# Optimization experiments

Hardware: AMD Instinct MI355X
Metric: run time of the kernel (lower is better)

The kernel has to match this reference:

```python
import jax, jax.numpy as jnp
import numpy as np

B, S, D = 4, 2048, 1024
H = 16
HD = D // H  # 64


def _xavier(key, shape):
    fan_in, fan_out = shape[1], shape[0]
    limit = float(np.sqrt(6.0 / (fan_in + fan_out)))
    return jax.random.uniform(key, shape, jnp.float32, -limit, limit)


def setup_inputs() -> dict:
    key = jax.random.key(0)
    ks = jax.random.split(key, 5)
    x = jax.random.normal(ks[0], (B, S, D), dtype=jnp.float32)
    # nn.Linear weights are [out, in]; biases zero-initialized
    Wq = _xavier(ks[1], (D, D)); bq = jnp.zeros((D,), jnp.float32)
    Wk = _xavier(ks[2], (D, D)); bk = jnp.zeros((D,), jnp.float32)
    Wv = _xavier(ks[3], (D, D)); bv = jnp.zeros((D,), jnp.float32)
    Wo = _xavier(ks[4], (D, D)); bo = jnp.zeros((D,), jnp.float32)
    return {"x": x, "Wq": Wq, "bq": bq, "Wk": Wk, "bk": bk,
            "Wv": Wv, "bv": bv, "Wo": Wo, "bo": bo}


def reference(x, Wq, bq, Wk, bk, Wv, bv, Wo, bo):
    # Projections (torch Linear: y = x @ W.T + b), reshape to [B, H, S, HD]
    def proj(W, b):
        y = jnp.einsum('bsd,ed->bse', x, W) + b
        return y.reshape(B, S, H, HD).transpose(0, 2, 1, 3)

    q = proj(Wq, bq)
    k = proj(Wk, bk)
    v = proj(Wv, bv)

    scale = 1.0 / jnp.sqrt(jnp.float32(HD))
    scores = jnp.einsum('bhqd,bhkd->bhqk', q, k) * scale  # [B,H,S,S]
    probs = jax.nn.softmax(scores, axis=-1)
    ctx = jnp.einsum('bhqk,bhkd->bhqd', probs, v)  # [B,H,S,HD]
    ctx = ctx.transpose(0, 2, 1, 3).reshape(B, S, D)
    out = jnp.einsum('bsd,ed->bse', ctx, Wo) + bo
    return out
```

## Files before the change

### kernel.cpp

```cpp
#include <hip/hip_runtime.h>
#include <hip/hip_bf16.h>
#include <stdint.h>


typedef __bf16 bf16;
typedef __bf16 bf16x8 __attribute__((ext_vector_type(8)));
typedef __bf16 bf16x4 __attribute__((ext_vector_type(4)));
typedef float  f32x4  __attribute__((ext_vector_type(4)));

#define MFMA_BF16(A, B, C) __builtin_amdgcn_mfma_f32_16x16x32_bf16(A, B, C, 0, 0, 0)
#define EXP2F(x) __builtin_amdgcn_exp2f(x)

#define ASYNC_CP16(DST_LDS, SRC_G)                                            \
  __builtin_amdgcn_global_load_lds(                                           \
      (__attribute__((address_space(1))) void*)(SRC_G),                       \
      (__attribute__((address_space(3))) void*)(DST_LDS), 16, 0, 0)

__global__ __launch_bounds__(256) void cvt5(
    const float* __restrict__ s0, bf16* __restrict__ d0, int n0,
    const float* __restrict__ s1, bf16* __restrict__ d1, int n1,
    const float* __restrict__ s2, bf16* __restrict__ d2, int n2,
    const float* __restrict__ s3, bf16* __restrict__ d3, int n3,
    const float* __restrict__ s4, bf16* __restrict__ d4, int n4)
{
  const float* s; bf16* d; int n;
  switch (blockIdx.y) {
    case 0: s = s0; d = d0; n = n0; break;
    case 1: s = s1; d = d1; n = n1; break;
    case 2: s = s2; d = d2; n = n2; break;
    case 3: s = s3; d = d3; n = n3; break;
    default: s = s4; d = d4; n = n4; break;
  }
  const int stride = gridDim.x * blockDim.x * 4;
  for (int i = (blockIdx.x * blockDim.x + threadIdx.x) * 4; i < n; i += stride) {
    const float4 v = *(const float4*)(s + i);
    bf16x4 o;
    o[0] = (bf16)v.x; o[1] = (bf16)v.y; o[2] = (bf16)v.z; o[3] = (bf16)v.w;
    *(bf16x4*)(d + i) = o;
  }
}

__global__ __launch_bounds__(256, 4) void gemm_qkv(
    const bf16* __restrict__ X,
    const bf16* __restrict__ Wq, const bf16* __restrict__ Wk,
    const bf16* __restrict__ Wv,
    const float* __restrict__ bq, const float* __restrict__ bk,
    const float* __restrict__ bv,
    bf16* __restrict__ Qo, bf16* __restrict__ Ko, bf16* __restrict__ Vo,
    float qscale)
{
  constexpr int N = 1024, K = 1024;
  __shared__ alignas(16) bf16 As[8192];
  __shared__ alignas(16) bf16 Bs[8192];

  const int sel = blockIdx.x >> 3;
  const bf16*  W    = (sel == 0) ? Wq : (sel == 1) ? Wk : Wv;
  const float* bias = (sel == 0) ? bq : (sel == 1) ? bk : bv;
  bf16*        Y    = (sel == 0) ? Qo : (sel == 1) ? Ko : Vo;
  const float scale = (sel == 0) ? qscale : 1.0f;

  const int tid  = threadIdx.x;
  const int lane = tid & 63;
  const int wv   = tid >> 6;
  const int l15  = lane & 15;
  const int quad = lane >> 4;
  const int wm   = (wv >> 1) * 64;
  const int wn   = (wv & 1) * 64;
  const int nbase = (blockIdx.x & 7) * 128;
  const int mbase = blockIdx.y * 128;

  f32x4 acc[4][4];
  #pragma unroll
  for (int i = 0; i < 4; ++i)
    #pragma unroll
    for (int j = 0; j < 4; ++j)
      acc[i][j] = (f32x4){0.f, 0.f, 0.f, 0.f};

  const int r8 = lane >> 3;
  const int oc = (lane & 7) ^ r8;
  const size_t lrowA = (size_t)(mbase + wv * 32 + r8);
  const size_t lrowB = (size_t)(nbase + wv * 32 + r8);

  for (int kb = 0; kb < K; kb += 64) {
    #pragma unroll
    for (int c = 0; c < 4; ++c) {
      ASYNC_CP16(As + (wv * 32 + c * 8) * 64, X + (lrowA + c * 8) * K + kb + oc * 8);
      ASYNC_CP16(Bs + (wv * 32 + c * 8) * 64, W + (lrowB + c * 8) * K + kb + oc * 8);
    }
    __syncthreads();
    #pragma unroll
    for (int ks = 0; ks < 2; ++ks) {
      bf16x8 af[4], bfr[4];
      #pragma unroll
      for (int t = 0; t < 4; ++t) {
        const int ma = wm + t * 16 + l15;
        af[t]  = *(const bf16x8*)(As + (ma * 8 + ((ks * 4 + quad) ^ (ma & 7))) * 8);
        const int nb = wn + t * 16 + l15;
        bfr[t] = *(const bf16x8*)(Bs + (nb * 8 + ((ks * 4 + quad) ^ (nb & 7))) * 8);
      }
      #pragma unroll
      for (int i = 0; i < 4; ++i)
        #pragma unroll
        for (int j = 0; j < 4; ++j)
          acc[i][j] = MFMA_BF16(af[i], bfr[j], acc[i][j]);
    }
    __syncthreads();
  }

  #pragma unroll
  for (int i = 0; i < 4; ++i) {
    const int row0 = mbase + wm + i * 16 + quad * 4;
    #pragma unroll
    for (int j = 0; j < 4; ++j) {
      const int col = nbase + wn + j * 16 + l15;
      const float bv2 = bias[col];
      #pragma unroll
      for (int r = 0; r < 4; ++r) {
        const float v = (acc[i][j][r] + bv2) * scale;
        const int row = row0 + r;
        if (sel != 2) {
          Y[(size_t)row * N + col] = (bf16)v;
        } else {
          const int bb = row >> 11, s  = row & 2047;
          const int hh = col >> 6,  hd = col & 63;
          Y[(size_t)(bb * 16 + hh) * (2048 * 64) + (size_t)(s >> 6) * 4096 +
            hd * 64 + (s & 63)] = (bf16)v;
        }
      }
    }
  }
}

__global__ __launch_bounds__(256) void gemm_o(
    const bf16* __restrict__ X, const bf16* __restrict__ W,
    const float* __restrict__ bias, float* __restrict__ Yf)
{
  constexpr int N = 1024, K = 1024;
  __shared__ alignas(16) bf16 As[8192];
  __shared__ alignas(16) bf16 Bs[8192];

  const int tid  = threadIdx.x;
  const int lane = tid & 63;
  const int wv   = tid >> 6;
  const int l15  = lane & 15;
  const int quad = lane >> 4;
  const int wm   = (wv >> 1) * 64;
  const int wn   = (wv & 1) * 64;
  const int nbase = blockIdx.x * 128;
  const int mbase = blockIdx.y * 128;

  f32x4 acc[4][4];
  #pragma unroll
  for (int i = 0; i < 4; ++i)
    #pragma unroll
    for (int j = 0; j < 4; ++j)
      acc[i][j] = (f32x4){0.f, 0.f, 0.f, 0.f};

  const int r8 = lane >> 3;
  const int oc = (lane & 7) ^ r8;
  const size_t lrowA = (size_t)(mbase + wv * 32 + r8);
  const size_t lrowB = (size_t)(nbase + wv * 32 + r8);

  for (int kb = 0; kb < K; kb += 64) {
    #pragma unroll
    for (int c = 0; c < 4; ++c) {
      ASYNC_CP16(As + (wv * 32 + c * 8) * 64, X + (lrowA + c * 8) * K + kb + oc * 8);
      ASYNC_CP16(Bs + (wv * 32 + c * 8) * 64, W + (lrowB + c * 8) * K + kb + oc * 8);
    }
    __syncthreads();
    #pragma unroll
    for (int ks = 0; ks < 2; ++ks) {
      bf16x8 af[4], bfr[4];
      #pragma unroll
      for (int t = 0; t < 4; ++t) {
        const int ma = wm + t * 16 + l15;
        af[t]  = *(const bf16x8*)(As + (ma * 8 + ((ks * 4 + quad) ^ (ma & 7))) * 8);
        const int nb = wn + t * 16 + l15;
        bfr[t] = *(const bf16x8*)(Bs + (nb * 8 + ((ks * 4 + quad) ^ (nb & 7))) * 8);
      }
      #pragma unroll
      for (int i = 0; i < 4; ++i)
        #pragma unroll
        for (int j = 0; j < 4; ++j)
          acc[i][j] = MFMA_BF16(af[i], bfr[j], acc[i][j]);
    }
    __syncthreads();
  }

  #pragma unroll
  for (int i = 0; i < 4; ++i) {
    const int row0 = mbase + wm + i * 16 + quad * 4;
    #pragma unroll
    for (int j = 0; j < 4; ++j) {
      const int col = nbase + wn + j * 16 + l15;
      const float bv2 = bias[col];
      #pragma unroll
      for (int r = 0; r < 4; ++r)
        Yf[(size_t)(row0 + r) * N + col] = acc[i][j][r] + bv2;
    }
  }
}

__global__ __launch_bounds__(256, 4) void attn(
    const bf16* __restrict__ Qb, const bf16* __restrict__ Kb,
    const bf16* __restrict__ Vt, bf16* __restrict__ Ob)
{
  constexpr int S = 2048, D = 1024;
  __shared__ alignas(16) bf16 Ks[2][4096];
  __shared__ alignas(16) bf16 Vs[2][4096];

  const int tid  = threadIdx.x;
  const int lane = tid & 63;
  const int wv   = tid >> 6;
  const int l15  = lane & 15;
  const int q0   = lane >> 4;
  const int b = blockIdx.z, h = blockIdx.y;
  const int qblk = blockIdx.x * 128 + wv * 32;

  bf16x8 qf[2][2];
  #pragma unroll
  for (int qt = 0; qt < 2; ++qt)
    #pragma unroll
    for (int dh = 0; dh < 2; ++dh)
      qf[qt][dh] = *(const bf16x8*)(
          Qb + (size_t)(b * S + qblk + qt * 16 + l15) * D + h * 64 + dh * 32 + q0 * 8);

  float lrun[2] = {0.f, 0.f};
  f32x4 o[4][2];
  #pragma unroll
  for (int ht = 0; ht < 4; ++ht)
    #pragma unroll
    for (int qt = 0; qt < 2; ++qt)
      o[ht][qt] = (f32x4){0.f, 0.f, 0.f, 0.f};

  const int r8a = lane >> 3;
  const int oc1 = (lane & 7) ^ (r8a & 3);
  const int oc2 = oc1 ^ 4;
  const int ov  = (lane & 7) ^ r8a;
  const bf16* kgw = Kb + (size_t)(b * S) * D + h * 64 + (size_t)(16 * wv) * D;
  const bf16* vgw = Vt + (size_t)(b * 16 + h) * (2048 * 64) + (16 * wv) * 64;

#define STAGE(KC, BUF)                                                        \
  {                                                                           \
    const bf16* ks = kgw + (size_t)(KC) * D;                                  \
    ASYNC_CP16(&Ks[BUF][wv * 1024],       ks + (size_t)r8a * D + oc1 * 8);    \
    ASYNC_CP16(&Ks[BUF][wv * 1024 + 512], ks + (size_t)(8 + r8a) * D + oc2 * 8);\
    const bf16* vs = vgw + (KC) * 64;                                         \
    ASYNC_CP16(&Vs[BUF][wv * 1024],       vs + r8a * 64 + ov * 8);            \
    ASYNC_CP16(&Vs[BUF][wv * 1024 + 512], vs + (8 + r8a) * 64 + ov * 8);      \
  }

  const int kla = 8 * (l15 >> 2) + (l15 & 3);
  const int swa = (l15 & 3) | (((l15 >> 2) & 1) << 2);
  const int swv = l15 & 7;

  STAGE(0, 0);

  for (int kc = 0, it = 0; kc < S; kc += 64, ++it) {
    const int cur = it & 1;
    __syncthreads();
    if (kc + 64 < S) STAGE(kc + 64, cur ^ 1);

    f32x4 sc[2][4];
    #pragma unroll
    for (int kt = 0; kt < 4; ++kt) {
      const int key = kla + 4 * (kt & 1) + 32 * (kt >> 1);
      const bf16x8 kf0 = *(const bf16x8*)(&Ks[cur][(key * 8 + (q0 ^ swa)) * 8]);
      const bf16x8 kf1 = *(const bf16x8*)(&Ks[cur][(key * 8 + ((q0 + 4) ^ swa)) * 8]);
      #pragma unroll
      for (int qt = 0; qt < 2; ++qt) {
        f32x4 s = MFMA_BF16(kf0, qf[qt][0], ((f32x4){0.f, 0.f, 0.f, 0.f}));
        sc[qt][kt] = MFMA_BF16(kf1, qf[qt][1], s);
      }
    }

    bf16x8 pb[2][2];
    #pragma unroll
    for (int qt = 0; qt < 2; ++qt) {
      float ps = 0.f;
      #pragma unroll
      for (int kt = 0; kt < 4; ++kt)
        #pragma unroll
        for (int r = 0; r < 4; ++r) {
          const float p = EXP2F(sc[qt][kt][r]);
          ps += p;
          pb[qt][kt >> 1][(kt & 1) * 4 + r] = (bf16)p;
        }
      lrun[qt] += ps;
    }

    #pragma unroll
    for (int ht = 0; ht < 4; ++ht) {
      const int row = ht * 16 + l15;
      const bf16x8 vf0 = *(const bf16x8*)(&Vs[cur][(row * 8 + (q0 ^ swv)) * 8]);
      const bf16x8 vf1 = *(const bf16x8*)(&Vs[cur][(row * 8 + ((q0 + 4) ^ swv)) * 8]);
      #pragma unroll
      for (int qt = 0; qt < 2; ++qt) {
        o[ht][qt] = MFMA_BF16(vf0, pb[qt][0], o[ht][qt]);
        o[ht][qt] = MFMA_BF16(vf1, pb[qt][1], o[ht][qt]);
      }
    }
  }
#undef STAGE

  #pragma unroll
  for (int qt = 0; qt < 2; ++qt) {
    float l = lrun[qt];
    l += __shfl_xor(l, 16, 64);
    l += __shfl_xor(l, 32, 64);
    const float inv = 1.0f / l;
    bf16* orow = Ob + (size_t)(b * S + qblk + qt * 16 + l15) * D + h * 64 + q0 * 4;
    #pragma unroll
    for (int ht = 0; ht < 4; ++ht) {
      bf16x4 w;
      w[0] = (bf16)(o[ht][qt][0] * inv);
      w[1] = (bf16)(o[ht][qt][1] * inv);
      w[2] = (bf16)(o[ht][qt][2] * inv);
      w[3] = (bf16)(o[ht][qt][3] * inv);
      *(bf16x4*)(orow + ht * 16) = w;
    }
  }
}

extern "C" void kernel_launch(void* const* d_in, const int* in_sizes, int n_in,
                              void* d_out, int out_size, void* d_ws, size_t ws_size,
                              hipStream_t stream)
{
  const float* x  = (const float*)d_in[0];
  const float* Wq = (const float*)d_in[1];
  const float* bq = (const float*)d_in[2];
  const float* Wk = (const float*)d_in[3];
  const float* bk = (const float*)d_in[4];
  const float* Wv = (const float*)d_in[5];
  const float* bv = (const float*)d_in[6];
  const float* Wo = (const float*)d_in[7];
  const float* bo = (const float*)d_in[8];
  float* out = (float*)d_out;

  const size_t NX = (size_t)8192 * 1024;
  const size_t NW = (size_t)1024 * 1024;

  bf16* xb  = (bf16*)d_ws;
  bf16* Wqb = xb  + NX;
  bf16* Wkb = Wqb + NW;
  bf16* Wvb = Wkb + NW;
  bf16* Wob = Wvb + NW;
  bf16* Qb  = Wob + NW;
  bf16* Kb  = Qb  + NX;
  bf16* Vt  = Kb  + NX;
  bf16* Ctx = Vt  + NX;

  const float QSCALE = 0.18033688011112042f;

  dim3 bc(256, 1, 1);
  hipLaunchKernelGGL(cvt5, dim3(1024, 5, 1), bc, 0, stream,
                     x, xb, (int)NX, Wq, Wqb, (int)NW, Wk, Wkb, (int)NW,
                     Wv, Wvb, (int)NW, Wo, Wob, (int)NW);

  hipLaunchKernelGGL(gemm_qkv, dim3(24, 64, 1), bc, 0, stream,
                     xb, Wqb, Wkb, Wvb, bq, bk, bv, Qb, Kb, Vt, QSCALE);

  hipLaunchKernelGGL(attn, dim3(16, 16, 4), bc, 0, stream, Qb, Kb, Vt, Ctx);

  hipLaunchKernelGGL(gemm_o, dim3(8, 64, 1), bc, 0, stream, Ctx, Wob, bo, out);
}
```

Before: 280.8 us.

## Load K/V fragments directly from global memory instead of LDS staging in attention

Removes the double-buffered LDS staging of K and V tiles (async global-to-LDS copies plus per-iteration barriers), and has each wave read its K and V MFMA fragments straight from global memory into registers. Blocks grow to 512 threads (8 waves, 256 queries) to improve L2/L1 reuse of the shared K/V, and s_setprio is raised around the MFMA/exp section. The score computation is fused with the exp per key tile. This drops the syncthreads and LDS traffic but makes every wave issue redundant global loads with no prefetch overlap, relying on caches and wave interleaving to hide latency.

Result: slower. 500.8 us (+78.4%).

```diff
diff --git a/kernel.cpp b/kernel.cpp
--- a/kernel.cpp
+++ b/kernel.cpp
@@ -201,13 +201,11 @@
   }
 }
 
-__global__ __launch_bounds__(256, 4) void attn(
+__global__ __launch_bounds__(512, 4) void attn(
     const bf16* __restrict__ Qb, const bf16* __restrict__ Kb,
     const bf16* __restrict__ Vt, bf16* __restrict__ Ob)
 {
   constexpr int S = 2048, D = 1024;
-  __shared__ alignas(16) bf16 Ks[2][4096];
-  __shared__ alignas(16) bf16 Vs[2][4096];
 
   const int tid  = threadIdx.x;
   const int lane = tid & 63;
@@ -215,7 +213,7 @@
   const int l15  = lane & 15;
   const int q0   = lane >> 4;
   const int b = blockIdx.z, h = blockIdx.y;
-  const int qblk = blockIdx.x * 128 + wv * 32;
+  const int qblk = blockIdx.x * 256 + wv * 32;
 
   bf16x8 qf[2][2];
   #pragma unroll
@@ -233,75 +231,59 @@
     for (int qt = 0; qt < 2; ++qt)
       o[ht][qt] = (f32x4){0.f, 0.f, 0.f, 0.f};
 
-  const int r8a = lane >> 3;
-  const int oc1 = (lane & 7) ^ (r8a & 3);
-  const int oc2 = oc1 ^ 4;
-  const int ov  = (lane & 7) ^ r8a;
-  const bf16* kgw = Kb + (size_t)(b * S) * D + h * 64 + (size_t)(16 * wv) * D;
-  const bf16* vgw = Vt + (size_t)(b * 16 + h) * (2048 * 64) + (16 * wv) * 64;
-
-#define STAGE(KC, BUF)                                                        \
-  {                                                                           \
-    const bf16* ks = kgw + (size_t)(KC) * D;                                  \
-    ASYNC_CP16(&Ks[BUF][wv * 1024],       ks + (size_t)r8a * D + oc1 * 8);    \
-    ASYNC_CP16(&Ks[BUF][wv * 1024 + 512], ks + (size_t)(8 + r8a) * D + oc2 * 8);\
-    const bf16* vs = vgw + (KC) * 64;                                         \
-    ASYNC_CP16(&Vs[BUF][wv * 1024],       vs + r8a * 64 + ov * 8);            \
-    ASYNC_CP16(&Vs[BUF][wv * 1024 + 512], vs + (8 + r8a) * 64 + ov * 8);      \
-  }
-
   const int kla = 8 * (l15 >> 2) + (l15 & 3);
-  const int swa = (l15 & 3) | (((l15 >> 2) & 1) << 2);
-  const int swv = l15 & 7;
-
-  STAGE(0, 0);
-
-  for (int kc = 0, it = 0; kc < S; kc += 64, ++it) {
-    const int cur = it & 1;
-    __syncthreads();
-    if (kc + 64 < S) STAGE(kc + 64, cur ^ 1);
-
-    f32x4 sc[2][4];
+  const bf16* kbase = Kb + (size_t)(b * S) * D + h * 64 + q0 * 8;
+  const bf16* vbase = Vt + (size_t)(b * 16 + h) * (2048 * 64) + q0 * 8;
+
+  for (int kc = 0; kc < S; kc += 64) {
+    bf16x8 kf[4][2];
     #pragma unroll
     for (int kt = 0; kt < 4; ++kt) {
-      const int key = kla + 4 * (kt & 1) + 32 * (kt >> 1);
-      const bf16x8 kf0 = *(const bf16x8*)(&Ks[cur][(key * 8 + (q0 ^ swa)) * 8]);
-      const bf16x8 kf1 = *(const bf16x8*)(&Ks[cur][(key * 8 + ((q0 + 4) ^ swa)) * 8]);
+      const bf16* kp =
+          kbase + (size_t)(kc + kla + 4 * (kt & 1) + 32 * (kt >> 1)) * D;
+      kf[kt][0] = *(const bf16x8*)(kp);
+      kf[kt][1] = *(const bf16x8*)(kp + 32);
+    }
+    bf16x8 vf[4][2];
+    const bf16* vp0 = vbase + (size_t)(kc >> 6) * 4096;
+    #pragma unroll
+    for (int ht = 0; ht < 4; ++ht) {
+      const bf16* vp = vp0 + (ht * 16 + l15) * 64;
+      vf[ht][0] = *(const bf16x8*)(vp);
+      vf[ht][1] = *(const bf16x8*)(vp + 32);
+    }
+
+    __builtin_amdgcn_s_setprio(1);
+
+    bf16x8 pb[2][2];
+    #pragma unroll
+    for (int kt = 0; kt < 4; ++kt) {
       #pragma unroll
       for (int qt = 0; qt < 2; ++qt) {
-        f32x4 s = MFMA_BF16(kf0, qf[qt][0], ((f32x4){0.f, 0.f, 0.f, 0.f}));
-        sc[qt][kt] = MFMA_BF16(kf1, qf[qt][1], s);
-      }
-    }
-
-    bf16x8 pb[2][2];
-    #pragma unroll
-    for (int qt = 0; qt < 2; ++qt) {
-      float ps = 0.f;
-      #pragma unroll
-      for (int kt = 0; kt < 4; ++kt)
+        f32x4 s = MFMA_BF16(kf[kt][0], qf[qt][0], ((f32x4){0.f, 0.f, 0.f, 0.f}));
+        s = MFMA_BF16(kf[kt][1], qf[qt][1], s);
+        float ps = 0.f;
         #pragma unroll
         for (int r = 0; r < 4; ++r) {
-          const float p = EXP2F(sc[qt][kt][r]);
+          const float p = EXP2F(s[r]);
           ps += p;
           pb[qt][kt >> 1][(kt & 1) * 4 + r] = (bf16)p;
         }
-      lrun[qt] += ps;
+        lrun[qt] += ps;
+      }
     }
 
     #pragma unroll
     for (int ht = 0; ht < 4; ++ht) {
-      const int row = ht * 16 + l15;
-      const bf16x8 vf0 = *(const bf16x8*)(&Vs[cur][(row * 8 + (q0 ^ swv)) * 8]);
-      const bf16x8 vf1 = *(const bf16x8*)(&Vs[cur][(row * 8 + ((q0 + 4) ^ swv)) * 8]);
       #pragma unroll
       for (int qt = 0; qt < 2; ++qt) {
-        o[ht][qt] = MFMA_BF16(vf0, pb[qt][0], o[ht][qt]);
-        o[ht][qt] = MFMA_BF16(vf1, pb[qt][1], o[ht][qt]);
-      }
-    }
-  }
-#undef STAGE
+        o[ht][qt] = MFMA_BF16(vf[ht][0], pb[qt][0], o[ht][qt]);
+        o[ht][qt] = MFMA_BF16(vf[ht][1], pb[qt][1], o[ht][qt]);
+      }
+    }
+
+    __builtin_amdgcn_s_setprio(0);
+  }
 
   #pragma unroll
   for (int qt = 0; qt < 2; ++qt) {
@@ -360,7 +342,8 @@
   hipLaunchKernelGGL(gemm_qkv, dim3(24, 64, 1), bc, 0, stream,
                      xb, Wqb, Wkb, Wvb, bq, bk, bv, Qb, Kb, Vt, QSCALE);
 
-  hipLaunchKernelGGL(attn, dim3(16, 16, 4), bc, 0, stream, Qb, Kb, Vt, Ctx);
+  hipLaunchKernelGGL(attn, dim3(8, 16, 4), dim3(512, 1, 1), 0, stream,
+                     Qb, Kb, Vt, Ctx);
 
   hipLaunchKernelGGL(gemm_o, dim3(8, 64, 1), bc, 0, stream, Ctx, Wob, bo, out);
 }
```
